# Performance work log

Hardware: AMD Instinct MI355X
Metric: run time of the kernel (lower is better)

## Reference

```python
import jax, jax.numpy as jnp
import numpy as np

N_NODES = 50000
N_EDGES = 1600000
N_FEAT = 128
HIDDEN = 128
N_GRAPHS = 64
N_CLASSES = 10
N_REGS = 1


def setup_inputs() -> dict:
    key = jax.random.key(0)
    ks = jax.random.split(key, 16)
    inp = {
        "x": jax.random.normal(ks[0], (N_NODES, N_FEAT), dtype=jnp.float32),
        "edge_index": jax.random.randint(ks[1], (2, N_EDGES), 0, N_NODES, dtype=jnp.int32),
        "batch": jnp.sort(jax.random.randint(ks[2], (N_NODES,), 0, N_GRAPHS, dtype=jnp.int32)),
        # GCNConv layer params (PyG: linear without bias applied first, bias added after aggregation)
        "w0": jax.random.normal(ks[3], (N_FEAT, HIDDEN), dtype=jnp.float32) * 0.05,
        "b0": jax.random.normal(ks[4], (HIDDEN,), dtype=jnp.float32) * 0.05,
        "w1": jax.random.normal(ks[5], (HIDDEN, HIDDEN), dtype=jnp.float32) * 0.05,
        "b1": jax.random.normal(ks[6], (HIDDEN,), dtype=jnp.float32) * 0.05,
        "w2": jax.random.normal(ks[7], (HIDDEN, HIDDEN), dtype=jnp.float32) * 0.05,
        "b2": jax.random.normal(ks[8], (HIDDEN,), dtype=jnp.float32) * 0.05,
        # heads
        "wc": jax.random.normal(ks[9], (HIDDEN, N_CLASSES), dtype=jnp.float32) * 0.05,
        "bc": jax.random.normal(ks[10], (N_CLASSES,), dtype=jnp.float32) * 0.05,
        "wr": jax.random.normal(ks[11], (HIDDEN, N_REGS), dtype=jnp.float32) * 0.05,
        "br": jax.random.normal(ks[12], (N_REGS,), dtype=jnp.float32) * 0.05,
    }
    return inp


def _gcn_layer(x, src, dst, w, b, deg_inv_sqrt, deg_inv):
    # x: [N, Din] -> [N, Dout]. GCNConv: D^-1/2 (A+I) D^-1/2 (x W) + b
    h = x @ w  # [N, Dout]
    coef = (deg_inv_sqrt[src] * deg_inv_sqrt[dst])[:, None]  # [E, 1]
    agg = jax.ops.segment_sum(h[src] * coef, dst, num_segments=x.shape[0])
    agg = agg + h * deg_inv[:, None]  # self-loop term: deg^-1 * h
    return agg + b


def reference(x, edge_index, batch, w0, b0, w1, b1, w2, b2, wc, bc, wr, br):
    src, dst = edge_index[0], edge_index[1]
    n = x.shape[0]
    # degrees include self-loop weight 1 (PyG gcn_norm with edge_weight=1)
    deg = jax.ops.segment_sum(jnp.ones(src.shape, x.dtype), dst, num_segments=n) + 1.0
    deg_inv_sqrt = deg ** -0.5
    deg_inv = 1.0 / deg

    h = _gcn_layer(x, src, dst, w0, b0, deg_inv_sqrt, deg_inv)
    h = _gcn_layer(jax.nn.elu(h), src, dst, w1, b1, deg_inv_sqrt, deg_inv)
    h = _gcn_layer(jax.nn.elu(h), src, dst, w2, b2, deg_inv_sqrt, deg_inv)

    # global mean pool over graphs
    sums = jax.ops.segment_sum(h, batch, num_segments=N_GRAPHS)  # [G, H]
    cnt = jax.ops.segment_sum(jnp.ones((n,), h.dtype), batch, num_segments=N_GRAPHS)
    pooled = sums / jnp.maximum(cnt, 1.0)[:, None]

    cls_out = pooled @ wc + bc
    reg_out = pooled @ wr + br
    return (pooled, cls_out, reg_out)
```

## Files before the change

### kernel.cpp

```cpp
#include <hip/hip_runtime.h>
#include <hip/hip_fp16.h>
#include <math.h>

#define N_NODES   50000
#define N_EDGES   1600000
#define NF        128
#define N_GRAPHS  64
#define N_CLASSES 10

#define NBK       391
#define BK_SHIFT  7
#define BK_NODES  128
#define SLAB      5120
#define CHUNK     4096
#define NCHUNKS   ((N_EDGES + CHUNK - 1) / CHUNK)

typedef _Float16 half8 __attribute__((ext_vector_type(8)));
typedef float f32x4 __attribute__((ext_vector_type(4)));

__global__ void k_zero(int* __restrict__ bucket_cur, float* __restrict__ sums) {
    int i = blockIdx.x * 256 + threadIdx.x;
    if (i < NBK) bucket_cur[i] = i * SLAB;
    if (i < N_GRAPHS * NF) sums[i] = 0.f;
}

__global__ __launch_bounds__(256) void k_bscatter(const int* __restrict__ src,
                                                  const int* __restrict__ dst,
                                                  int* __restrict__ bucket_cur,
                                                  int* __restrict__ pairs) {
    __shared__ int h[NBK], rb[NBK], c2[NBK];
    int t = threadIdx.x;
    for (int i = t; i < NBK; i += 256) { h[i] = 0; c2[i] = 0; }
    __syncthreads();
    int base = blockIdx.x * CHUNK;
    int end = min(base + CHUNK, N_EDGES);
    for (int e = base + t; e < end; e += 256)
        atomicAdd(&h[dst[e] >> BK_SHIFT], 1);
    __syncthreads();
    for (int i = t; i < NBK; i += 256)
        rb[i] = h[i] ? atomicAdd(&bucket_cur[i], h[i]) : 0;
    __syncthreads();
    for (int e = base + t; e < end; e += 256) {
        int d = dst[e];
        int b = d >> BK_SHIFT;
        int k = atomicAdd(&c2[b], 1);
        pairs[rb[b] + k] = (src[e] << BK_SHIFT) | (d & (BK_NODES - 1));
    }
}

__global__ __launch_bounds__(512) void k_bfill(const int* __restrict__ pairs,
                                               const int* __restrict__ bucket_cur,
                                               int* __restrict__ row_start,
                                               int* __restrict__ row_end,
                                               float* __restrict__ dis,
                                               int* __restrict__ csr_src) {
    __shared__ int cnt[BK_NODES];
    __shared__ int cur[BK_NODES];
    __shared__ int ts[512];
    int b = blockIdx.x, t = threadIdx.x;
    int node_base = b << BK_SHIFT;
    int lo = b * SLAB, hi = bucket_cur[b];

    if (t < BK_NODES) cnt[t] = 0;
    __syncthreads();
    for (int e = lo + t; e < hi; e += 512)
        atomicAdd(&cnt[pairs[e] & (BK_NODES - 1)], 1);
    __syncthreads();

    int a = (t < BK_NODES) ? cnt[t] : 0;
    ts[t] = a;
    __syncthreads();
    for (int off = 1; off < BK_NODES; off <<= 1) {
        int y = (t >= off) ? ts[t - off] : 0;
        __syncthreads();
        ts[t] += y;
        __syncthreads();
    }
    int row = lo + ts[t] - a;
    if (t < BK_NODES) {
        cur[t] = row;
        int n = node_base + t;
        if (n < N_NODES) {
            row_start[n] = row;
            row_end[n]   = row + a;
            dis[n] = rsqrtf((float)(a + 1));
        }
    }
    __syncthreads();

    for (int e = lo + t; e < hi; e += 512) {
        int p = pairs[e];
        int pos = atomicAdd(&cur[p & (BK_NODES - 1)], 1);
        csr_src[pos] = p >> BK_SHIFT;
    }
}

__global__ void k_wconv(const float* __restrict__ w0, const float* __restrict__ w1,
                        const float* __restrict__ w2, _Float16* __restrict__ wf) {
    int b = blockIdx.x, t = threadIdx.x;
    const float* W = (b == 0) ? w0 : (b == 1) ? w1 : w2;
    _Float16* dst = wf + (size_t)b * NF * NF;
    for (int idx = t; idx < NF * NF; idx += 256) {
        int k = idx >> 7, n = idx & 127;
        int nt = n >> 4, kc = k >> 5, quad = (k >> 3) & 3, j = k & 7;
        int lane = quad * 16 + (n & 15);
        dst[((nt * 4 + kc) * 64 + lane) * 8 + j] = (_Float16)W[idx];
    }
}

template <bool ELU, bool FP32IN>
__global__ __launch_bounds__(256) void k_gemm(const void* __restrict__ Xv,
                                              const _Float16* __restrict__ WF,
                                              const float* __restrict__ dis,
                                              __half* __restrict__ H) {
    __shared__ _Float16 xs[64 * 136];
    const _Float16* Xh = (const _Float16*)Xv;
    const float*    Xf = (const float*)Xv;
    int t = threadIdx.x;
    int row0 = blockIdx.x * 64;
#pragma unroll
    for (int i = 0; i < 4; i++) {
        int f = i * 256 + t;
        int r = f >> 4, c = (f & 15) * 8;
        int gr = row0 + r;
        half8 v = {};
        if (gr < N_NODES) {
            if (FP32IN) {
                float4 v0 = *(const float4*)&Xf[(size_t)gr * NF + c];
                float4 v1 = *(const float4*)&Xf[(size_t)gr * NF + c + 4];
                v[0] = (_Float16)v0.x; v[1] = (_Float16)v0.y;
                v[2] = (_Float16)v0.z; v[3] = (_Float16)v0.w;
                v[4] = (_Float16)v1.x; v[5] = (_Float16)v1.y;
                v[6] = (_Float16)v1.z; v[7] = (_Float16)v1.w;
            } else {
                v = *(const half8*)&Xh[(size_t)gr * NF + c];
            }
        }
        if (ELU) {
#pragma unroll
            for (int j = 0; j < 8; j++) {
                float xv = (float)v[j];
                v[j] = (_Float16)(xv > 0.f ? xv : (expf(xv) - 1.f));
            }
        }
        *(half8*)&xs[r * 136 + c] = v;
    }
    __syncthreads();

    int w = t >> 6;
    int lane = t & 63;
    int m = lane & 15, quad = lane >> 4;

    half8 a[4];
#pragma unroll
    for (int kc = 0; kc < 4; kc++)
        a[kc] = *(const half8*)&xs[(w * 16 + m) * 136 + kc * 32 + quad * 8];

    f32x4 acc[8];
#pragma unroll
    for (int nt = 0; nt < 8; nt++) {
        f32x4 c4 = {0.f, 0.f, 0.f, 0.f};
#pragma unroll
        for (int kc = 0; kc < 4; kc++) {
            half8 bf = *(const half8*)&WF[((nt * 4 + kc) * 64 + lane) * 8];
            c4 = __builtin_amdgcn_mfma_f32_16x16x32_f16(a[kc], bf, c4, 0, 0, 0);
        }
        acc[nt] = c4;
    }

    __syncthreads();
#pragma unroll
    for (int reg = 0; reg < 4; reg++) {
        int r = w * 16 + quad * 4 + reg;
        int gr = row0 + r;
        float ds = (gr < N_NODES) ? dis[gr] : 0.f;
#pragma unroll
        for (int nt = 0; nt < 8; nt++)
            xs[r * 136 + nt * 16 + m] = (_Float16)(ds * acc[nt][reg]);
    }
    __syncthreads();
#pragma unroll
    for (int i = 0; i < 4; i++) {
        int f = i * 256 + t;
        int r = f >> 4, c = (f & 15) * 8;
        int gr = row0 + r;
        if (gr < N_NODES)
            *(half8*)&H[(size_t)gr * NF + c] = *(const half8*)&xs[r * 136 + c];
    }
}

template <bool POOL>
__global__ __launch_bounds__(256) void k_agg(const __half* __restrict__ H,
                                             const float* __restrict__ bias,
                                             const int* __restrict__ row_start,
                                             const int* __restrict__ row_end,
                                             const int* __restrict__ csr_src,
                                             const float* __restrict__ dis,
                                             const int* __restrict__ batch,
                                             void* __restrict__ outv) {
    __shared__ float pacc[NF];
    const uint2* H4 = (const uint2*)H;
    int t = threadIdx.x;
    int lane = t & 63;
    int node = blockIdx.x * 8 + (t >> 6) * 2 + (lane >> 5);
    int l    = lane & 31;
    int c    = l * 4;
    if (POOL) {
        if (t < NF) pacc[t] = 0.f;
        __syncthreads();
    }
    float o0 = 0.f, o1 = 0.f, o2 = 0.f, o3 = 0.f;
    bool active = node < N_NODES;
    if (active) {
        int rs = row_start[node], re = row_end[node];
        float a0 = 0.f, a1 = 0.f, a2 = 0.f, a3 = 0.f;
        int e = rs;
        for (; e + 7 < re; e += 8) {
            uint2 v[8];
#pragma unroll
            for (int j = 0; j < 8; j++) {
                int s = csr_src[e + j];
                v[j] = H4[(size_t)s * 32 + l];
            }
#pragma unroll
            for (int j = 0; j < 8; j++) {
                float2 lo = __half22float2(*(__half2*)&v[j].x);
                float2 hi = __half22float2(*(__half2*)&v[j].y);
                a0 += lo.x; a1 += lo.y; a2 += hi.x; a3 += hi.y;
            }
        }
        for (; e < re; e++) {
            int s = csr_src[e];
            uint2 v = H4[(size_t)s * 32 + l];
            float2 lo = __half22float2(*(__half2*)&v.x);
            float2 hi = __half22float2(*(__half2*)&v.y);
            a0 += lo.x; a1 += lo.y; a2 += hi.x; a3 += hi.y;
        }
        {
            uint2 v = H4[(size_t)node * 32 + l];
            float2 lo = __half22float2(*(__half2*)&v.x);
            float2 hi = __half22float2(*(__half2*)&v.y);
            a0 += lo.x; a1 += lo.y; a2 += hi.x; a3 += hi.y;
        }
        float di = dis[node];
        float4 bv = *(const float4*)&bias[c];
        o0 = a0 * di + bv.x; o1 = a1 * di + bv.y;
        o2 = a2 * di + bv.z; o3 = a3 * di + bv.w;
        if (!POOL) {
            uint2 o;
            *(__half2*)&o.x = __floats2half2_rn(o0, o1);
            *(__half2*)&o.y = __floats2half2_rn(o2, o3);
            ((uint2*)outv)[(size_t)node * 32 + l] = o;
        }
    }
    if (POOL) {
        float* sums = (float*)outv;
        int first = blockIdx.x * 8;
        int last  = min(first + 7, N_NODES - 1);
        int g0 = batch[first], g7 = batch[last];
        if (active) {
            if (g0 == g7) {
                atomicAdd(&pacc[c + 0], o0);
                atomicAdd(&pacc[c + 1], o1);
                atomicAdd(&pacc[c + 2], o2);
                atomicAdd(&pacc[c + 3], o3);
            } else {
                int g = batch[node];
                atomicAdd(&sums[g * NF + c + 0], o0);
                atomicAdd(&sums[g * NF + c + 1], o1);
                atomicAdd(&sums[g * NF + c + 2], o2);
                atomicAdd(&sums[g * NF + c + 3], o3);
            }
        }
        __syncthreads();
        if (t < NF && g0 == g7) atomicAdd(&sums[g0 * NF + t], pacc[t]);
    }
}

__global__ void k_head(const float* __restrict__ sums, const int* __restrict__ batch,
                       const float* __restrict__ wc, const float* __restrict__ bc,
                       const float* __restrict__ wr, const float* __restrict__ br,
                       float* __restrict__ out) {
    __shared__ float p[128];
    __shared__ int cnt_s;
    int g = blockIdx.x, c = threadIdx.x;
    if (c == 0) {
        int lo = 0, hi = N_NODES;
        while (lo < hi) { int m = (lo + hi) >> 1; if (batch[m] < g) lo = m + 1; else hi = m; }
        int s0 = lo;
        lo = 0; hi = N_NODES;
        while (lo < hi) { int m = (lo + hi) >> 1; if (batch[m] < g + 1) lo = m + 1; else hi = m; }
        cnt_s = lo - s0;
    }
    __syncthreads();
    float cnt = (float)max(cnt_s, 1);
    float pv = sums[g * NF + c] / cnt;
    p[c] = pv;
    out[g * NF + c] = pv;
    __syncthreads();
    if (c < N_CLASSES) {
        float d = bc[c];
        for (int k = 0; k < NF; k++) d += p[k] * wc[k * N_CLASSES + c];
        out[N_GRAPHS * NF + g * N_CLASSES + c] = d;
    }
    if (c == N_CLASSES) {
        float d = br[0];
        for (int k = 0; k < NF; k++) d += p[k] * wr[k];
        out[N_GRAPHS * NF + N_GRAPHS * N_CLASSES + g] = d;
    }
}

extern "C" void kernel_launch(void* const* d_in, const int* in_sizes, int n_in,
                              void* d_out, int out_size, void* d_ws, size_t ws_size,
                              hipStream_t stream) {
    const float* x     = (const float*)d_in[0];
    const int*   ei    = (const int*)d_in[1];
    const int*   batch = (const int*)d_in[2];
    const float* w0 = (const float*)d_in[3];
    const float* b0 = (const float*)d_in[4];
    const float* w1 = (const float*)d_in[5];
    const float* b1 = (const float*)d_in[6];
    const float* w2 = (const float*)d_in[7];
    const float* b2 = (const float*)d_in[8];
    const float* wc = (const float*)d_in[9];
    const float* bc = (const float*)d_in[10];
    const float* wr = (const float*)d_in[11];
    const float* br = (const float*)d_in[12];
    const int* srcp = ei;
    const int* dstp = ei + N_EDGES;
    float* out = (float*)d_out;

    char* ws = (char*)d_ws;
    size_t off = 0;
    auto alloc = [&](size_t bytes) -> void* {
        void* p = ws + off;
        off = (off + bytes + 255) & ~(size_t)255;
        return p;
    };
    int*      row_start  = (int*)alloc(N_NODES * 4);
    int*      row_end    = (int*)alloc(N_NODES * 4);
    int*      bucket_cur = (int*)alloc(NBK * 4);
    float*    dis        = (float*)alloc(N_NODES * 4);
    int*      csr_src    = (int*)alloc((size_t)NBK * SLAB * 4);
    __half*   Hbuf       = (__half*)alloc((size_t)N_NODES * NF * 2);
    _Float16* Ah         = (_Float16*)alloc((size_t)N_NODES * NF * 2);
    _Float16* wf         = (_Float16*)alloc((size_t)3 * NF * NF * 2);
    float*    sums       = (float*)alloc(N_GRAPHS * NF * 4);
    (void)ws_size;
    int* pairs = (int*)Hbuf;

    k_zero<<<32, 256, 0, stream>>>(bucket_cur, sums);
    k_bscatter<<<NCHUNKS, 256, 0, stream>>>(srcp, dstp, bucket_cur, pairs);
    k_bfill<<<NBK, 512, 0, stream>>>(pairs, bucket_cur, row_start, row_end, dis, csr_src);
    k_wconv<<<3, 256, 0, stream>>>(w0, w1, w2, wf);

    const int gemm_grid = (N_NODES + 63) / 64;
    const int agg_grid  = (N_NODES + 7) / 8;

    k_gemm<false, true><<<gemm_grid, 256, 0, stream>>>(x, wf, dis, Hbuf);
    k_agg<false><<<agg_grid, 256, 0, stream>>>(Hbuf, b0, row_start, row_end, csr_src, dis, batch, Ah);
    k_gemm<true, false><<<gemm_grid, 256, 0, stream>>>(Ah, wf + NF * NF, dis, Hbuf);
    k_agg<false><<<agg_grid, 256, 0, stream>>>(Hbuf, b1, row_start, row_end, csr_src, dis, batch, Ah);
    k_gemm<true, false><<<gemm_grid, 256, 0, stream>>>(Ah, wf + 2 * NF * NF, dis, Hbuf);
    k_agg<true><<<agg_grid, 256, 0, stream>>>(Hbuf, b2, row_start, row_end, csr_src, dis, batch, sums);

    k_head<<<N_GRAPHS, 128, 0, stream>>>(sums, batch, wc, bc, wr, br, out);
}
```

Baseline: 376.5 us.

## Store features in four 32-column slices and aggregate one slice per block

The hidden feature matrix moves from row-major to a slice-major layout with four contiguous 32-feature slices. The GEMM reads and writes that layout, and the aggregation kernel handles one slice per block, with block indices interleaved so that neighbouring blocks work on different slices. The goal is to shrink the gather working set per pass so that random neighbour rows stay in L2/MALL. The cost is that every slice block reads csr_src again (4x index traffic), and the edge loop is now predicated with nontemporal loads and stores. The pooling reduction is also changed to wave shuffles over 32-node blocks.

```diff
diff --git a/kernel.cpp b/kernel.cpp
--- a/kernel.cpp
+++ b/kernel.cpp
@@ -14,6 +14,12 @@
 #define SLAB      5120
 #define CHUNK     4096
 #define NCHUNKS   ((N_EDGES + CHUNK - 1) / CHUNK)
+
+#define NSLICE    4
+#define SLICE_F   32
+#define AGG_NPB   32
+#define AGG_NPS   1563
+#define AGG_GRID  (8 * 782)
 
 typedef _Float16 half8 __attribute__((ext_vector_type(8)));
 typedef float f32x4 __attribute__((ext_vector_type(4)));
@@ -133,7 +139,7 @@
                 v[4] = (_Float16)v1.x; v[5] = (_Float16)v1.y;
                 v[6] = (_Float16)v1.z; v[7] = (_Float16)v1.w;
             } else {
-                v = *(const half8*)&Xh[(size_t)gr * NF + c];
+                v = *(const half8*)&Xh[((size_t)(c >> 5) * N_NODES + gr) * 32 + (c & 31)];
             }
         }
         if (ELU) {
@@ -185,7 +191,8 @@
         int r = f >> 4, c = (f & 15) * 8;
         int gr = row0 + r;
         if (gr < N_NODES)
-            *(half8*)&H[(size_t)gr * NF + c] = *(const half8*)&xs[r * 136 + c];
+            *(half8*)&H[((size_t)(c >> 5) * N_NODES + gr) * 32 + (c & 31)] =
+                *(const half8*)&xs[r * 136 + c];
     }
 }
 
@@ -198,30 +205,36 @@
                                              const float* __restrict__ dis,
                                              const int* __restrict__ batch,
                                              void* __restrict__ outv) {
-    __shared__ float pacc[NF];
-    const uint2* H4 = (const uint2*)H;
+    __shared__ float pacc[SLICE_F];
+    int r8    = blockIdx.x & 7;
+    int q     = blockIdx.x >> 3;
+    int slice = r8 >> 1;
+    int nb    = q * 2 + (r8 & 1);
+    if (nb >= AGG_NPS) return;
     int t = threadIdx.x;
-    int lane = t & 63;
-    int node = blockIdx.x * 8 + (t >> 6) * 2 + (lane >> 5);
-    int l    = lane & 31;
-    int c    = l * 4;
+    int grp = t >> 3;
+    int l   = t & 7;
+    int node = nb * AGG_NPB + grp;
+    bool active = node < N_NODES;
+    const uint2* Hs = (const uint2*)H + (size_t)slice * N_NODES * 8;
+
     if (POOL) {
-        if (t < NF) pacc[t] = 0.f;
+        if (t < SLICE_F) pacc[t] = 0.f;
         __syncthreads();
     }
-    float o0 = 0.f, o1 = 0.f, o2 = 0.f, o3 = 0.f;
-    bool active = node < N_NODES;
+
+    float a0 = 0.f, a1 = 0.f, a2 = 0.f, a3 = 0.f;
     if (active) {
         int rs = row_start[node], re = row_end[node];
-        float a0 = 0.f, a1 = 0.f, a2 = 0.f, a3 = 0.f;
-        int e = rs;
-        for (; e + 7 < re; e += 8) {
+        for (int e = rs; e < re; e += 8) {
+            int  s[8];
             uint2 v[8];
 #pragma unroll
-            for (int j = 0; j < 8; j++) {
-                int s = csr_src[e + j];
-                v[j] = H4[(size_t)s * 32 + l];
-            }
+            for (int j = 0; j < 8; j++)
+                s[j] = (e + j < re) ? __builtin_nontemporal_load(&csr_src[e + j]) : -1;
+#pragma unroll
+            for (int j = 0; j < 8; j++)
+                v[j] = (s[j] >= 0) ? Hs[(size_t)s[j] * 8 + l] : make_uint2(0u, 0u);
 #pragma unroll
             for (int j = 0; j < 8; j++) {
                 float2 lo = __half22float2(*(__half2*)&v[j].x);
@@ -229,51 +242,57 @@
                 a0 += lo.x; a1 += lo.y; a2 += hi.x; a3 += hi.y;
             }
         }
-        for (; e < re; e++) {
-            int s = csr_src[e];
-            uint2 v = H4[(size_t)s * 32 + l];
+        {
+            uint2 v = Hs[(size_t)node * 8 + l];
             float2 lo = __half22float2(*(__half2*)&v.x);
             float2 hi = __half22float2(*(__half2*)&v.y);
             a0 += lo.x; a1 += lo.y; a2 += hi.x; a3 += hi.y;
         }
-        {
-            uint2 v = H4[(size_t)node * 32 + l];
-            float2 lo = __half22float2(*(__half2*)&v.x);
-            float2 hi = __half22float2(*(__half2*)&v.y);
-            a0 += lo.x; a1 += lo.y; a2 += hi.x; a3 += hi.y;
-        }
+    }
+
+    float o0 = 0.f, o1 = 0.f, o2 = 0.f, o3 = 0.f;
+    if (active) {
         float di = dis[node];
-        float4 bv = *(const float4*)&bias[c];
+        float4 bv = *(const float4*)&bias[slice * SLICE_F + l * 4];
         o0 = a0 * di + bv.x; o1 = a1 * di + bv.y;
         o2 = a2 * di + bv.z; o3 = a3 * di + bv.w;
         if (!POOL) {
-            uint2 o;
-            *(__half2*)&o.x = __floats2half2_rn(o0, o1);
-            *(__half2*)&o.y = __floats2half2_rn(o2, o3);
-            ((uint2*)outv)[(size_t)node * 32 + l] = o;
-        }
-    }
+            union { unsigned long long u; struct { __half2 lo, hi; } h; } pk;
+            pk.h.lo = __floats2half2_rn(o0, o1);
+            pk.h.hi = __floats2half2_rn(o2, o3);
+            __builtin_nontemporal_store(pk.u,
+                &((unsigned long long*)outv)[((size_t)slice * N_NODES + node) * 8 + l]);
+        }
+    }
+
     if (POOL) {
         float* sums = (float*)outv;
-        int first = blockIdx.x * 8;
-        int last  = min(first + 7, N_NODES - 1);
-        int g0 = batch[first], g7 = batch[last];
-        if (active) {
-            if (g0 == g7) {
-                atomicAdd(&pacc[c + 0], o0);
-                atomicAdd(&pacc[c + 1], o1);
-                atomicAdd(&pacc[c + 2], o2);
-                atomicAdd(&pacc[c + 3], o3);
-            } else {
-                int g = batch[node];
-                atomicAdd(&sums[g * NF + c + 0], o0);
-                atomicAdd(&sums[g * NF + c + 1], o1);
-                atomicAdd(&sums[g * NF + c + 2], o2);
-                atomicAdd(&sums[g * NF + c + 3], o3);
+        int first = nb * AGG_NPB;
+        int last  = min(first + AGG_NPB - 1, N_NODES - 1);
+        int g0 = batch[first], gl = batch[last];
+        if (g0 == gl) {
+            o0 += __shfl_xor(o0, 8);  o1 += __shfl_xor(o1, 8);
+            o2 += __shfl_xor(o2, 8);  o3 += __shfl_xor(o3, 8);
+            o0 += __shfl_xor(o0, 16); o1 += __shfl_xor(o1, 16);
+            o2 += __shfl_xor(o2, 16); o3 += __shfl_xor(o3, 16);
+            o0 += __shfl_xor(o0, 32); o1 += __shfl_xor(o1, 32);
+            o2 += __shfl_xor(o2, 32); o3 += __shfl_xor(o3, 32);
+            if ((t & 63) < 8) {
+                atomicAdd(&pacc[l * 4 + 0], o0);
+                atomicAdd(&pacc[l * 4 + 1], o1);
+                atomicAdd(&pacc[l * 4 + 2], o2);
+                atomicAdd(&pacc[l * 4 + 3], o3);
             }
-        }
-        __syncthreads();
-        if (t < NF && g0 == g7) atomicAdd(&sums[g0 * NF + t], pacc[t]);
+            __syncthreads();
+            if (t < SLICE_F)
+                atomicAdd(&sums[g0 * NF + slice * SLICE_F + t], pacc[t]);
+        } else if (active) {
+            int g = batch[node];
+            atomicAdd(&sums[g * NF + slice * SLICE_F + l * 4 + 0], o0);
+            atomicAdd(&sums[g * NF + slice * SLICE_F + l * 4 + 1], o1);
+            atomicAdd(&sums[g * NF + slice * SLICE_F + l * 4 + 2], o2);
+            atomicAdd(&sums[g * NF + slice * SLICE_F + l * 4 + 3], o3);
+        }
     }
 }
 
@@ -355,14 +374,13 @@
     k_wconv<<<3, 256, 0, stream>>>(w0, w1, w2, wf);
 
     const int gemm_grid = (N_NODES + 63) / 64;
-    const int agg_grid  = (N_NODES + 7) / 8;
 
     k_gemm<false, true><<<gemm_grid, 256, 0, stream>>>(x, wf, dis, Hbuf);
-    k_agg<false><<<agg_grid, 256, 0, stream>>>(Hbuf, b0, row_start, row_end, csr_src, dis, batch, Ah);
+    k_agg<false><<<AGG_GRID, 256, 0, stream>>>(Hbuf, b0, row_start, row_end, csr_src, dis, batch, Ah);
     k_gemm<true, false><<<gemm_grid, 256, 0, stream>>>(Ah, wf + NF * NF, dis, Hbuf);
-    k_agg<false><<<agg_grid, 256, 0, stream>>>(Hbuf, b1, row_start, row_end, csr_src, dis, batch, Ah);
+    k_agg<false><<<AGG_GRID, 256, 0, stream>>>(Hbuf, b1, row_start, row_end, csr_src, dis, batch, Ah);
     k_gemm<true, false><<<gemm_grid, 256, 0, stream>>>(Ah, wf + 2 * NF * NF, dis, Hbuf);
-    k_agg<true><<<agg_grid, 256, 0, stream>>>(Hbuf, b2, row_start, row_end, csr_src, dis, batch, sums);
+    k_agg<true><<<AGG_GRID, 256, 0, stream>>>(Hbuf, b2, row_start, row_end, csr_src, dis, batch, sums);
 
     k_head<<<N_GRAPHS, 128, 0, stream>>>(sums, batch, wc, bc, wr, br, out);
 }
```

Measured after the change: 484.5 us. +28.7%, slower.

## Widen aggregation gathers to 16-byte loads with 16 lanes per node and prefetch indices

Applied to the files above, without the earlier changes.

The aggregation kernel now gives each node 16 lanes that each load 16 bytes (uint4, 8 halves) instead of 32 lanes loading 8 bytes, so each block covers 16 nodes. The next batch of 8 csr_src indices is prefetched while the current batch of rows is gathered, which hides index-load latency. In the pooling variant, partial sums are first reduced across the four nodes in a wavefront with shuffles, which cuts shared-memory atomics. The costs are more accumulator registers per lane and possibly lower occupancy.

```diff
diff --git a/kernel.cpp b/kernel.cpp
--- a/kernel.cpp
+++ b/kernel.cpp
@@ -14,6 +14,9 @@
 #define SLAB      5120
 #define CHUNK     4096
 #define NCHUNKS   ((N_EDGES + CHUNK - 1) / CHUNK)
+
+#define AGG_NPB   16
+#define AGG_GRID  ((N_NODES + AGG_NPB - 1) / AGG_NPB)
 
 typedef _Float16 half8 __attribute__((ext_vector_type(8)));
 typedef float f32x4 __attribute__((ext_vector_type(4)));
@@ -199,81 +202,123 @@
                                              const int* __restrict__ batch,
                                              void* __restrict__ outv) {
     __shared__ float pacc[NF];
-    const uint2* H4 = (const uint2*)H;
+    const uint4* H16 = (const uint4*)H;
     int t = threadIdx.x;
-    int lane = t & 63;
-    int node = blockIdx.x * 8 + (t >> 6) * 2 + (lane >> 5);
-    int l    = lane & 31;
-    int c    = l * 4;
+    int node = blockIdx.x * AGG_NPB + (t >> 4);
+    int l    = t & 15;
+    bool active = node < N_NODES;
+
     if (POOL) {
         if (t < NF) pacc[t] = 0.f;
         __syncthreads();
     }
-    float o0 = 0.f, o1 = 0.f, o2 = 0.f, o3 = 0.f;
-    bool active = node < N_NODES;
+
+    float a[8] = {0.f, 0.f, 0.f, 0.f, 0.f, 0.f, 0.f, 0.f};
     if (active) {
         int rs = row_start[node], re = row_end[node];
-        float a0 = 0.f, a1 = 0.f, a2 = 0.f, a3 = 0.f;
         int e = rs;
-        for (; e + 7 < re; e += 8) {
-            uint2 v[8];
-#pragma unroll
-            for (int j = 0; j < 8; j++) {
-                int s = csr_src[e + j];
-                v[j] = H4[(size_t)s * 32 + l];
-            }
-#pragma unroll
-            for (int j = 0; j < 8; j++) {
-                float2 lo = __half22float2(*(__half2*)&v[j].x);
-                float2 hi = __half22float2(*(__half2*)&v[j].y);
-                a0 += lo.x; a1 += lo.y; a2 += hi.x; a3 += hi.y;
+        if (e + 7 < re) {
+            int s[8];
+#pragma unroll
+            for (int j = 0; j < 8; j++) s[j] = csr_src[e + j];
+            for (; e + 15 < re; e += 8) {
+                int sn[8];
+#pragma unroll
+                for (int j = 0; j < 8; j++) sn[j] = csr_src[e + 8 + j];
+                uint4 v[8];
+#pragma unroll
+                for (int j = 0; j < 8; j++) v[j] = H16[(size_t)s[j] * 16 + l];
+#pragma unroll
+                for (int j = 0; j < 8; j++) {
+                    float2 f0 = __half22float2(*(__half2*)&v[j].x);
+                    float2 f1 = __half22float2(*(__half2*)&v[j].y);
+                    float2 f2 = __half22float2(*(__half2*)&v[j].z);
+                    float2 f3 = __half22float2(*(__half2*)&v[j].w);
+                    a[0] += f0.x; a[1] += f0.y; a[2] += f1.x; a[3] += f1.y;
+                    a[4] += f2.x; a[5] += f2.y; a[6] += f3.x; a[7] += f3.y;
+                }
+#pragma unroll
+                for (int j = 0; j < 8; j++) s[j] = sn[j];
+            }
+            {
+                uint4 v[8];
+#pragma unroll
+                for (int j = 0; j < 8; j++) v[j] = H16[(size_t)s[j] * 16 + l];
+#pragma unroll
+                for (int j = 0; j < 8; j++) {
+                    float2 f0 = __half22float2(*(__half2*)&v[j].x);
+                    float2 f1 = __half22float2(*(__half2*)&v[j].y);
+                    float2 f2 = __half22float2(*(__half2*)&v[j].z);
+                    float2 f3 = __half22float2(*(__half2*)&v[j].w);
+                    a[0] += f0.x; a[1] += f0.y; a[2] += f1.x; a[3] += f1.y;
+                    a[4] += f2.x; a[5] += f2.y; a[6] += f3.x; a[7] += f3.y;
+                }
+                e += 8;
             }
         }
         for (; e < re; e++) {
-            int s = csr_src[e];
-            uint2 v = H4[(size_t)s * 32 + l];
-            float2 lo = __half22float2(*(__half2*)&v.x);
-            float2 hi = __half22float2(*(__half2*)&v.y);
-            a0 += lo.x; a1 += lo.y; a2 += hi.x; a3 += hi.y;
+            uint4 v = H16[(size_t)csr_src[e] * 16 + l];
+            float2 f0 = __half22float2(*(__half2*)&v.x);
+            float2 f1 = __half22float2(*(__half2*)&v.y);
+            float2 f2 = __half22float2(*(__half2*)&v.z);
+            float2 f3 = __half22float2(*(__half2*)&v.w);
+            a[0] += f0.x; a[1] += f0.y; a[2] += f1.x; a[3] += f1.y;
+            a[4] += f2.x; a[5] += f2.y; a[6] += f3.x; a[7] += f3.y;
         }
         {
-            uint2 v = H4[(size_t)node * 32 + l];
-            float2 lo = __half22float2(*(__half2*)&v.x);
-            float2 hi = __half22float2(*(__half2*)&v.y);
-            a0 += lo.x; a1 += lo.y; a2 += hi.x; a3 += hi.y;
-        }
+            uint4 v = H16[(size_t)node * 16 + l];
+            float2 f0 = __half22float2(*(__half2*)&v.x);
+            float2 f1 = __half22float2(*(__half2*)&v.y);
+            float2 f2 = __half22float2(*(__half2*)&v.z);
+            float2 f3 = __half22float2(*(__half2*)&v.w);
+            a[0] += f0.x; a[1] += f0.y; a[2] += f1.x; a[3] += f1.y;
+            a[4] += f2.x; a[5] += f2.y; a[6] += f3.x; a[7] += f3.y;
+        }
+    }
+
+    float o[8] = {0.f, 0.f, 0.f, 0.f, 0.f, 0.f, 0.f, 0.f};
+    if (active) {
         float di = dis[node];
-        float4 bv = *(const float4*)&bias[c];
-        o0 = a0 * di + bv.x; o1 = a1 * di + bv.y;
-        o2 = a2 * di + bv.z; o3 = a3 * di + bv.w;
+        float4 b0 = *(const float4*)&bias[l * 8];
+        float4 b1 = *(const float4*)&bias[l * 8 + 4];
+        o[0] = a[0] * di + b0.x; o[1] = a[1] * di + b0.y;
+        o[2] = a[2] * di + b0.z; o[3] = a[3] * di + b0.w;
+        o[4] = a[4] * di + b1.x; o[5] = a[5] * di + b1.y;
+        o[6] = a[6] * di + b1.z; o[7] = a[7] * di + b1.w;
         if (!POOL) {
-            uint2 o;
-            *(__half2*)&o.x = __floats2half2_rn(o0, o1);
-            *(__half2*)&o.y = __floats2half2_rn(o2, o3);
-            ((uint2*)outv)[(size_t)node * 32 + l] = o;
-        }
-    }
+            uint4 pk;
+            *(__half2*)&pk.x = __floats2half2_rn(o[0], o[1]);
+            *(__half2*)&pk.y = __floats2half2_rn(o[2], o[3]);
+            *(__half2*)&pk.z = __floats2half2_rn(o[4], o[5]);
+            *(__half2*)&pk.w = __floats2half2_rn(o[6], o[7]);
+            ((uint4*)outv)[(size_t)node * 16 + l] = pk;
+        }
+    }
+
     if (POOL) {
         float* sums = (float*)outv;
-        int first = blockIdx.x * 8;
-        int last  = min(first + 7, N_NODES - 1);
-        int g0 = batch[first], g7 = batch[last];
-        if (active) {
-            if (g0 == g7) {
-                atomicAdd(&pacc[c + 0], o0);
-                atomicAdd(&pacc[c + 1], o1);
-                atomicAdd(&pacc[c + 2], o2);
-                atomicAdd(&pacc[c + 3], o3);
-            } else {
-                int g = batch[node];
-                atomicAdd(&sums[g * NF + c + 0], o0);
-                atomicAdd(&sums[g * NF + c + 1], o1);
-                atomicAdd(&sums[g * NF + c + 2], o2);
-                atomicAdd(&sums[g * NF + c + 3], o3);
-            }
-        }
-        __syncthreads();
-        if (t < NF && g0 == g7) atomicAdd(&sums[g0 * NF + t], pacc[t]);
+        int first = blockIdx.x * AGG_NPB;
+        int last  = min(first + AGG_NPB - 1, N_NODES - 1);
+        int g0 = batch[first], gl = batch[last];
+        if (g0 == gl) {
+#pragma unroll
+            for (int k = 0; k < 8; k++) {
+                o[k] += __shfl_xor(o[k], 16);
+                o[k] += __shfl_xor(o[k], 32);
+            }
+            if ((t & 63) < 16) {
+#pragma unroll
+                for (int k = 0; k < 8; k++)
+                    atomicAdd(&pacc[l * 8 + k], o[k]);
+            }
+            __syncthreads();
+            if (t < NF) atomicAdd(&sums[g0 * NF + t], pacc[t]);
+        } else if (active) {
+            int g = batch[node];
+#pragma unroll
+            for (int k = 0; k < 8; k++)
+                atomicAdd(&sums[g * NF + l * 8 + k], o[k]);
+        }
     }
 }
 
@@ -355,14 +400,13 @@
     k_wconv<<<3, 256, 0, stream>>>(w0, w1, w2, wf);
 
     const int gemm_grid = (N_NODES + 63) / 64;
-    const int agg_grid  = (N_NODES + 7) / 8;
 
     k_gemm<false, true><<<gemm_grid, 256, 0, stream>>>(x, wf, dis, Hbuf);
-    k_agg<false><<<agg_grid, 256, 0, stream>>>(Hbuf, b0, row_start, row_end, csr_src, dis, batch, Ah);
+    k_agg<false><<<AGG_GRID, 256, 0, stream>>>(Hbuf, b0, row_start, row_end, csr_src, dis, batch, Ah);
     k_gemm<true, false><<<gemm_grid, 256, 0, stream>>>(Ah, wf + NF * NF, dis, Hbuf);
-    k_agg<false><<<agg_grid, 256, 0, stream>>>(Hbuf, b1, row_start, row_end, csr_src, dis, batch, Ah);
+    k_agg<false><<<AGG_GRID, 256, 0, stream>>>(Hbuf, b1, row_start, row_end, csr_src, dis, batch, Ah);
     k_gemm<true, false><<<gemm_grid, 256, 0, stream>>>(Ah, wf + 2 * NF * NF, dis, Hbuf);
-    k_agg<true><<<agg_grid, 256, 0, stream>>>(Hbuf, b2, row_start, row_end, csr_src, dis, batch, sums);
+    k_agg<true><<<AGG_GRID, 256, 0, stream>>>(Hbuf, b2, row_start, row_end, csr_src, dis, batch, sums);
 
     k_head<<<N_GRAPHS, 128, 0, stream>>>(sums, batch, wc, bc, wr, br, out);
 }
```

After: 360.4 us. 1.04x faster.
